# Optimization experiments

Measured on AMD Instinct MI355X. Metric: run time of the kernel, lower is better.

Reference implementation:

```python
import jax, jax.numpy as jnp
import numpy as np

TEMPERATURE = 0.1
BASE_TEMPERATURE = 1.0
LAMBDA_PROTOTYPE = 1.0
EPS = 1e-12  # F.normalize eps

N, C, D, P = 65536, 128, 512, 128


def setup_inputs() -> dict:
    key = jax.random.key(0)
    k1, k2, k3, k4, k5 = jax.random.split(key, 5)
    return {
        "outputs": jax.random.normal(k1, (N, C), dtype=jnp.float32),
        "targets": jax.random.normal(k2, (N, C), dtype=jnp.float32),
        "backbone_features": jax.random.normal(k3, (N, D), dtype=jnp.float32),
        "prototype_features": jax.random.normal(k4, (P, D), dtype=jnp.float32),
        "prototype_labels": jax.random.randint(k5, (N, P), 0, 2, dtype=jnp.int32),
        "prototype_weights": jnp.ones((P,), dtype=jnp.float32),
    }


def reference(outputs, targets, backbone_features, prototype_features,
              prototype_labels, prototype_weights):
    # L2-normalize backbone features along feature dim (F.normalize, dim=1)
    norm = jnp.maximum(jnp.linalg.norm(backbone_features, axis=1, keepdims=True), EPS)
    bf = backbone_features / norm  # (N, D)

    n = outputs.reshape(-1, outputs.shape[-1]).shape[0]

    # Batched version of the per-sample loop: one GEMM for all samples.
    logits = jnp.einsum('nd,pd->np', bf, prototype_features) / TEMPERATURE  # (N, P)
    # Per-sample max subtraction for stability (detached in torch)
    logits = logits - jax.lax.stop_gradient(jnp.max(logits, axis=1, keepdims=True))

    mask = prototype_labels.astype(logits.dtype) * prototype_weights  # (N, P)
    exp_logits = jnp.exp(logits) * (1.0 - mask)
    log_prob = logits - jnp.log(jnp.sum(exp_logits, axis=1, keepdims=True))  # (N, P)
    mean_log_prob_pos = jnp.sum(mask * log_prob, axis=1)  # (N,)

    ctr_loss = -(TEMPERATURE / BASE_TEMPERATURE) * mean_log_prob_pos
    loss = jnp.sum(ctr_loss) / n
    return LAMBDA_PROTOTYPE * loss
```

## Files before the change

kernel.cpp:

```cpp
#include <hip/hip_runtime.h>
#include <hip/hip_bf16.h>
#include <math.h>

typedef __bf16 bf16x8v __attribute__((ext_vector_type(8)));
typedef __bf16 bf16x4v __attribute__((ext_vector_type(4)));
typedef float  f32x4   __attribute__((ext_vector_type(4)));

#define D_DIM 512
#define P_DIM 128
#define LDB   520
#define TEMP  0.1f
#define ROWS_PER_BLOCK 256
#define THREADS 1024

__global__ __launch_bounds__(THREADS, 4)
void mrc_fused(const float* __restrict__ bfeat,
               const float* __restrict__ protos,
               const int*   __restrict__ labels,
               const float* __restrict__ weights,
               float*       __restrict__ out,
               int nrows)
{
    __shared__ __bf16 sB[P_DIM * LDB];
    __shared__ float  sRed[16];

    const int t    = threadIdx.x;
    const int lane = t & 63;
    const int wave = t >> 6;
    const int q    = lane >> 4;
    const int cl   = lane & 15;

    const long long r0 = (long long)blockIdx.x * ROWS_PER_BLOCK + wave * 16;

    int lab[4][8];
    {
        const int* lbase = labels + r0 * (long long)P_DIM;
#pragma unroll
        for (int reg = 0; reg < 4; ++reg)
#pragma unroll
            for (int ct = 0; ct < 8; ++ct)
                lab[reg][ct] = __builtin_nontemporal_load(
                    lbase + (q * 4 + reg) * P_DIM + ct * 16 + cl);
    }

#pragma unroll
    for (int i = 0; i < 16; ++i) {
        const int f   = i * THREADS + t;
        const int row = f >> 7;
        const int c4  = f & 127;
        const f32x4 v = *(const f32x4*)(protos + row * D_DIM + c4 * 4);
        bf16x4v b;
        b[0] = (__bf16)v[0]; b[1] = (__bf16)v[1]; b[2] = (__bf16)v[2]; b[3] = (__bf16)v[3];
        *(bf16x4v*)&sB[row * LDB + c4 * 4] = b;
    }
    __syncthreads();

    const float* arow = bfeat + (r0 + cl) * (long long)D_DIM + q * 8;

    float wcol[8];
#pragma unroll
    for (int ct = 0; ct < 8; ++ct) wcol[ct] = weights[ct * 16 + cl];

    f32x4 acc[8];
#pragma unroll
    for (int ct = 0; ct < 8; ++ct) acc[ct] = (f32x4){0.f, 0.f, 0.f, 0.f};

    float ss = 0.f;
    f32x4 p[2][2];
    p[0][0] = __builtin_nontemporal_load((const f32x4*)(arow));
    p[0][1] = __builtin_nontemporal_load((const f32x4*)(arow + 4));
    p[1][0] = __builtin_nontemporal_load((const f32x4*)(arow + 32));
    p[1][1] = __builtin_nontemporal_load((const f32x4*)(arow + 36));

#pragma unroll 4
    for (int ks = 0; ks < 16; ++ks) {
        const f32x4 c0 = p[ks & 1][0], c1 = p[ks & 1][1];
        if (ks < 14) {
            p[ks & 1][0] = __builtin_nontemporal_load((const f32x4*)(arow + (ks + 2) * 32));
            p[ks & 1][1] = __builtin_nontemporal_load((const f32x4*)(arow + (ks + 2) * 32 + 4));
        }
        ss += c0[0]*c0[0] + c0[1]*c0[1] + c0[2]*c0[2] + c0[3]*c0[3]
            + c1[0]*c1[0] + c1[1]*c1[1] + c1[2]*c1[2] + c1[3]*c1[3];
        bf16x8v af;
        af[0]=(__bf16)c0[0]; af[1]=(__bf16)c0[1]; af[2]=(__bf16)c0[2]; af[3]=(__bf16)c0[3];
        af[4]=(__bf16)c1[0]; af[5]=(__bf16)c1[1]; af[6]=(__bf16)c1[2]; af[7]=(__bf16)c1[3];
        const int k0 = ks * 32 + q * 8;
#pragma unroll
        for (int ct = 0; ct < 8; ++ct) {
            const bf16x8v bfr = *(const bf16x8v*)&sB[(ct * 16 + cl) * LDB + k0];
            acc[ct] = __builtin_amdgcn_mfma_f32_16x16x32_bf16(af, bfr, acc[ct], 0, 0, 0);
        }
    }

    ss += __shfl_xor(ss, 16);
    ss += __shfl_xor(ss, 32);
    const float scale = 1.0f / (fmaxf(sqrtf(ss), 1e-12f) * TEMP);

    float pos_acc = 0.f;
#pragma unroll
    for (int reg = 0; reg < 4; ++reg) {
        const float rscale = __shfl(scale, q * 4 + reg, 16);
        float lg[8];
        float m = -3.4e38f;
#pragma unroll
        for (int ct = 0; ct < 8; ++ct) {
            lg[ct] = acc[ct][reg] * rscale;
            m = fmaxf(m, lg[ct]);
        }
        m = fmaxf(m, __shfl_xor(m, 1, 16));
        m = fmaxf(m, __shfl_xor(m, 2, 16));
        m = fmaxf(m, __shfl_xor(m, 4, 16));
        m = fmaxf(m, __shfl_xor(m, 8, 16));

        float s = 0.f, pz = 0.f, msum = 0.f;
#pragma unroll
        for (int ct = 0; ct < 8; ++ct) {
            const float mask = (float)lab[reg][ct] * wcol[ct];
            const float z = lg[ct] - m;
            s    += __expf(z) * (1.0f - mask);
            pz   += mask * z;
            msum += mask;
        }
        s += __shfl_xor(s, 1, 16);
        s += __shfl_xor(s, 2, 16);
        s += __shfl_xor(s, 4, 16);
        s += __shfl_xor(s, 8, 16);
        pos_acc += pz - logf(s) * msum;
    }

    pos_acc += __shfl_xor(pos_acc, 1);
    pos_acc += __shfl_xor(pos_acc, 2);
    pos_acc += __shfl_xor(pos_acc, 4);
    pos_acc += __shfl_xor(pos_acc, 8);
    pos_acc += __shfl_xor(pos_acc, 16);
    pos_acc += __shfl_xor(pos_acc, 32);
    if (lane == 0) sRed[wave] = pos_acc;
    __syncthreads();
    if (t == 0) {
        float total = 0.f;
#pragma unroll
        for (int w = 0; w < 16; ++w) total += sRed[w];
        atomicAdd(out, total * (-TEMP / (float)nrows));
    }
}

extern "C" void kernel_launch(void* const* d_in, const int* in_sizes, int n_in,
                              void* d_out, int out_size, void* d_ws, size_t ws_size,
                              hipStream_t stream) {
    const float* bfeat   = (const float*)d_in[2];
    const float* protos  = (const float*)d_in[3];
    const int*   labels  = (const int*)d_in[4];
    const float* weights = (const float*)d_in[5];
    float* out = (float*)d_out;

    const int nrows = in_sizes[2] / D_DIM;

    hipMemsetAsync(d_out, 0, sizeof(float) * out_size, stream);
    const int nblocks = nrows / ROWS_PER_BLOCK;
    mrc_fused<<<nblocks, THREADS, 0, stream>>>(bfeat, protos, labels, weights, out, nrows);
}
```

Before: 255.7 us.

## Defer label loads into the K loop and deepen the feature prefetch

Label loads are moved from the kernel prologue into the K loop, issued at iterations 12 and 14, so they no longer sit in registers during the whole GEMM and overlap with the final MFMAs. The A-row prefetch is deepened from two to three stages and the loop is fully unrolled. The prototype staging now converts eight elements per thread with 16-byte LDS stores, the sum of squares is split into two accumulators, and logf becomes __logf. Register pressure may rise from the deeper prefetch and full unroll, which could reduce occupancy under the 1024-thread launch bounds.

```diff
diff --git a/kernel.cpp b/kernel.cpp
--- a/kernel.cpp
+++ b/kernel.cpp
@@ -32,30 +32,22 @@
 
     const long long r0 = (long long)blockIdx.x * ROWS_PER_BLOCK + wave * 16;
 
-    int lab[4][8];
-    {
-        const int* lbase = labels + r0 * (long long)P_DIM;
 #pragma unroll
-        for (int reg = 0; reg < 4; ++reg)
-#pragma unroll
-            for (int ct = 0; ct < 8; ++ct)
-                lab[reg][ct] = __builtin_nontemporal_load(
-                    lbase + (q * 4 + reg) * P_DIM + ct * 16 + cl);
-    }
-
-#pragma unroll
-    for (int i = 0; i < 16; ++i) {
+    for (int i = 0; i < 8; ++i) {
         const int f   = i * THREADS + t;
-        const int row = f >> 7;
-        const int c4  = f & 127;
-        const f32x4 v = *(const f32x4*)(protos + row * D_DIM + c4 * 4);
-        bf16x4v b;
-        b[0] = (__bf16)v[0]; b[1] = (__bf16)v[1]; b[2] = (__bf16)v[2]; b[3] = (__bf16)v[3];
-        *(bf16x4v*)&sB[row * LDB + c4 * 4] = b;
+        const int row = f >> 6;
+        const int c8  = f & 63;
+        const f32x4 v0 = *(const f32x4*)(protos + row * D_DIM + c8 * 8);
+        const f32x4 v1 = *(const f32x4*)(protos + row * D_DIM + c8 * 8 + 4);
+        bf16x8v b;
+        b[0] = (__bf16)v0[0]; b[1] = (__bf16)v0[1]; b[2] = (__bf16)v0[2]; b[3] = (__bf16)v0[3];
+        b[4] = (__bf16)v1[0]; b[5] = (__bf16)v1[1]; b[6] = (__bf16)v1[2]; b[7] = (__bf16)v1[3];
+        *(bf16x8v*)&sB[row * LDB + c8 * 8] = b;
     }
     __syncthreads();
 
-    const float* arow = bfeat + (r0 + cl) * (long long)D_DIM + q * 8;
+    const float* arow  = bfeat + (r0 + cl) * (long long)D_DIM + q * 8;
+    const int*   lbase = labels + r0 * (long long)P_DIM + q * 4 * P_DIM + cl;
 
     float wcol[8];
 #pragma unroll
@@ -65,22 +57,39 @@
 #pragma unroll
     for (int ct = 0; ct < 8; ++ct) acc[ct] = (f32x4){0.f, 0.f, 0.f, 0.f};
 
-    float ss = 0.f;
-    f32x4 p[2][2];
-    p[0][0] = __builtin_nontemporal_load((const f32x4*)(arow));
-    p[0][1] = __builtin_nontemporal_load((const f32x4*)(arow + 4));
-    p[1][0] = __builtin_nontemporal_load((const f32x4*)(arow + 32));
-    p[1][1] = __builtin_nontemporal_load((const f32x4*)(arow + 36));
+    f32x4 pa[3], pb[3];
+#pragma unroll
+    for (int i = 0; i < 3; ++i) {
+        pa[i] = __builtin_nontemporal_load((const f32x4*)(arow + i * 32));
+        pb[i] = __builtin_nontemporal_load((const f32x4*)(arow + i * 32 + 4));
+    }
 
-#pragma unroll 4
+    int lab[4][8];
+    float ss0 = 0.f, ss1 = 0.f;
+
+#pragma unroll
     for (int ks = 0; ks < 16; ++ks) {
-        const f32x4 c0 = p[ks & 1][0], c1 = p[ks & 1][1];
-        if (ks < 14) {
-            p[ks & 1][0] = __builtin_nontemporal_load((const f32x4*)(arow + (ks + 2) * 32));
-            p[ks & 1][1] = __builtin_nontemporal_load((const f32x4*)(arow + (ks + 2) * 32 + 4));
+        const f32x4 c0 = pa[ks % 3], c1 = pb[ks % 3];
+        if (ks < 13) {
+            pa[ks % 3] = __builtin_nontemporal_load((const f32x4*)(arow + (ks + 3) * 32));
+            pb[ks % 3] = __builtin_nontemporal_load((const f32x4*)(arow + (ks + 3) * 32 + 4));
         }
-        ss += c0[0]*c0[0] + c0[1]*c0[1] + c0[2]*c0[2] + c0[3]*c0[3]
-            + c1[0]*c1[0] + c1[1]*c1[1] + c1[2]*c1[2] + c1[3]*c1[3];
+        if (ks == 12) {
+#pragma unroll
+            for (int reg = 0; reg < 2; ++reg)
+#pragma unroll
+                for (int ct = 0; ct < 8; ++ct)
+                    lab[reg][ct] = __builtin_nontemporal_load(lbase + reg * P_DIM + ct * 16);
+        }
+        if (ks == 14) {
+#pragma unroll
+            for (int reg = 2; reg < 4; ++reg)
+#pragma unroll
+                for (int ct = 0; ct < 8; ++ct)
+                    lab[reg][ct] = __builtin_nontemporal_load(lbase + reg * P_DIM + ct * 16);
+        }
+        ss0 += c0[0]*c0[0] + c0[1]*c0[1] + c0[2]*c0[2] + c0[3]*c0[3];
+        ss1 += c1[0]*c1[0] + c1[1]*c1[1] + c1[2]*c1[2] + c1[3]*c1[3];
         bf16x8v af;
         af[0]=(__bf16)c0[0]; af[1]=(__bf16)c0[1]; af[2]=(__bf16)c0[2]; af[3]=(__bf16)c0[3];
         af[4]=(__bf16)c1[0]; af[5]=(__bf16)c1[1]; af[6]=(__bf16)c1[2]; af[7]=(__bf16)c1[3];
@@ -92,6 +101,7 @@
         }
     }
 
+    float ss = ss0 + ss1;
     ss += __shfl_xor(ss, 16);
     ss += __shfl_xor(ss, 32);
     const float scale = 1.0f / (fmaxf(sqrtf(ss), 1e-12f) * TEMP);
@@ -125,7 +135,7 @@
         s += __shfl_xor(s, 2, 16);
         s += __shfl_xor(s, 4, 16);
         s += __shfl_xor(s, 8, 16);
-        pos_acc += pz - logf(s) * msum;
+        pos_acc += pz - __logf(s) * msum;
     }
 
     pos_acc += __shfl_xor(pos_acc, 1);
```

Result: faster. 240.6 us (-5.9%).
